# Kernel tuning notes

Measured on AMD Instinct MI355X. Metric: run time of the kernel, lower is better.

The kernel has to match this reference:

```python
import jax, jax.numpy as jnp
import numpy as np
from jax import lax

# Rotation permutations for a flattened 3x3 kernel (row-major, new_flat[t] = orig_flat[perm[t]]),
# transcribed literally from _rotate_kernel for n = angle//45 in {0,1,2,3}.
PERMS = np.array([
    [0, 1, 2, 3, 4, 5, 6, 7, 8],  # 0 deg (identity)
    [3, 0, 1, 6, 4, 2, 7, 8, 5],  # 45 deg: outer ring shifted one step
    [6, 3, 0, 7, 4, 1, 8, 5, 2],  # 90 deg clockwise
    [7, 6, 3, 8, 4, 0, 5, 2, 1],  # 135 deg
], dtype=np.int32)


def setup_inputs() -> dict:
    key = jax.random.key(0)
    k1, k2, k3 = jax.random.split(key, 3)
    B, Cin, Cout, H, W = 16, 64, 64, 128, 128
    x = jax.random.normal(k1, (B, Cin, H, W), dtype=jnp.float32)
    weight = jax.random.normal(k2, (Cout, Cin, 3, 3), dtype=jnp.float32)
    bias = jax.random.normal(k3, (Cout, 1, 1), dtype=jnp.float32)
    return {"x": x, "weight": weight, "bias": bias}


def reference(x, weight, bias):
    # x: [B, Cin, H, W]; weight: [Cout, Cin, 3, 3]; bias: [Cout, 1, 1]
    B, Cin, H, W = x.shape
    Cout = weight.shape[0]
    n_ang = PERMS.shape[0]

    # Build the 4 rotated kernel variants in one gather.
    wflat = weight.reshape(Cout, Cin, 9)
    # [Cout, Cin, n_ang, 9] -> [n_ang, Cout, Cin, 3, 3] -> merge angle into output channels
    wrot = wflat[:, :, jnp.asarray(PERMS)].transpose(2, 0, 1, 3).reshape(n_ang * Cout, Cin, 3, 3)

    # ZeroPad2d(stride=1) then valid 3x3 conv -> same spatial size.
    xp = jnp.pad(x, ((0, 0), (0, 0), (1, 1), (1, 1)))
    y = lax.conv_general_dilated(
        xp, wrot, window_strides=(1, 1), padding="VALID",
        dimension_numbers=("NCHW", "OIHW", "NCHW"))  # [B, n_ang*Cout, H, W]

    y = y.reshape(B, n_ang, Cout, H, W).transpose(1, 0, 2, 3, 4)  # [n_ang, B, Cout, H, W]
    return y + bias  # bias (Cout,1,1) broadcasts over trailing dims
```

## Files before the change

kernel.cpp:

```cpp
#include <hip/hip_runtime.h>


#define CIN 64
#define COUT 64
#define HH 128
#define WW 128
#define NB 16

typedef short bf16x8 __attribute__((ext_vector_type(8)));
typedef float f32x16 __attribute__((ext_vector_type(16)));

#define XS_SLOT 1072
#define XS_ROW  8576
#define XS_OFF  73728
#define LDS_BYTES (XS_OFF + 4 * XS_ROW)

__device__ __constant__ unsigned BOFF_d[4][9] = {
  {0,16,32,8576,8592,8608,17152,17168,17184},
  {16,32,8608,0,8592,17184,8576,17152,17168},
  {32,8608,17184,16,8592,17168,0,8576,17152},
  {8608,17184,17168,32,8592,17152,16,0,8576},
};

static __device__ __forceinline__ unsigned short f2bf(float f) {
  unsigned u = __builtin_bit_cast(unsigned, f);
  unsigned r = (u + 0x7FFFu + ((u >> 16) & 1u)) >> 16;
  return (unsigned short)r;
}

__global__ void build_A_kernel(const float* __restrict__ wgt,
                               unsigned short* __restrict__ A) {
  const int e = blockIdx.x * 256 + threadIdx.x;
  const int j = e & 7;
  const int cm = (e >> 3) & 63;
  const int half = (e >> 9) & 1;
  const int kc = e >> 10;
  const int s = kc >> 2, q = kc & 3;
  const int ci = q * 16 + half * 8 + j;
  A[e] = f2bf(wgt[(cm * CIN + ci) * 9 + s]);
}

__global__ __launch_bounds__(512) void aconv_persist_kernel(
    const float* __restrict__ x,
    const unsigned short* __restrict__ Ag,
    const float* __restrict__ bias,
    float* __restrict__ out)
{
  __shared__ __align__(16) unsigned char lds[LDS_BYTES];

  const int tid = threadIdx.x;
  const int lane = tid & 63;
  const int wid = tid >> 6;
  const int a   = wid >> 1;
  const int row = wid & 1;
  const int half = lane >> 5;
  const int ln = lane & 31;

  const int blk = blockIdx.x;
  const int b   = blk >> 4;
  const int rem = blk & 15;

  float bv[2][16];
  #pragma unroll
  for (int mf = 0; mf < 2; ++mf)
    #pragma unroll
    for (int g = 0; g < 16; ++g)
      bv[mf][g] = bias[mf * 32 + (g & 3) + 8 * (g >> 2) + 4 * half];

  unsigned boff[9];
  #pragma unroll
  for (int s = 0; s < 9; ++s) boff[s] = BOFF_d[a][s];

  {
    const uint4* Ag4 = (const uint4*)Ag;
    uint4* As4 = (uint4*)lds;
    #pragma unroll
    for (int i = 0; i < 9; ++i)
      As4[tid + i * 512] = Ag4[tid + i * 512];
  }

  int grr[5], gwI[5]; unsigned gdst[5]; const float* gxb[5];
  #pragma unroll
  for (int i = 0; i < 5; ++i) {
    const int g = tid + i * 512;
    const int gg = (g < 2112) ? g : 0;
    const int r = gg / 528;
    const int rest = gg - r * 528;
    const int slot = rest / 66;
    const int wI = rest - slot * 66;
    grr[i] = r; gwI[i] = wI;
    gdst[i] = (unsigned)(r * XS_ROW + slot * XS_SLOT + wI * 16);
    gxb[i] = x + (size_t)(b * CIN + slot * 8) * (HH * WW);
  }

  float gxv[5][8];

  {
    const int h0 = (rem * 4) * 2;
    const int w0 = 0;
    #pragma unroll
    for (int i = 0; i < 5; ++i) {
      const int g = tid + i * 512;
      const int gh = h0 - 1 + grr[i];
      const int gw = w0 - 1 + gwI[i];
      const bool inb = (g < 2112) && (gh >= 0) && (gh < HH) && (gw >= 0) && (gw < WW);
      const float* xp = gxb[i] + gh * WW + gw;
      #pragma unroll
      for (int q = 0; q < 8; ++q)
        gxv[i][q] = inb ? xp[q * (HH * WW)] : 0.f;
    }
    #pragma unroll
    for (int i = 0; i < 5; ++i)
      if (tid + i * 512 < 2112) {
        uint4 u4;
        u4.x = (unsigned)f2bf(gxv[i][0]) | ((unsigned)f2bf(gxv[i][1]) << 16);
        u4.y = (unsigned)f2bf(gxv[i][2]) | ((unsigned)f2bf(gxv[i][3]) << 16);
        u4.z = (unsigned)f2bf(gxv[i][4]) | ((unsigned)f2bf(gxv[i][5]) << 16);
        u4.w = (unsigned)f2bf(gxv[i][6]) | ((unsigned)f2bf(gxv[i][7]) << 16);
        *(uint4*)(lds + XS_OFF + gdst[i]) = u4;
      }
  }
  __syncthreads();

  const unsigned char* Asb = lds + (unsigned)(half * 1024 + ln * 16);
  const unsigned char* Bsb = lds + XS_OFF + (unsigned)(row * XS_ROW + half * XS_SLOT + ln * 16);

  for (int it = 0; it < 8; ++it) {
    const int h0 = (rem * 4 + (it >> 1)) * 2;
    const int w0 = (it & 1) * 64;

    if (it < 7) {
      const int itn = it + 1;
      const int h0n = (rem * 4 + (itn >> 1)) * 2;
      const int w0n = (itn & 1) * 64;
      #pragma unroll
      for (int i = 0; i < 5; ++i) {
        const int g = tid + i * 512;
        const int gh = h0n - 1 + grr[i];
        const int gw = w0n - 1 + gwI[i];
        const bool inb = (g < 2112) && (gh >= 0) && (gh < HH) && (gw >= 0) && (gw < WW);
        const float* xp = gxb[i] + gh * WW + gw;
        #pragma unroll
        for (int q = 0; q < 8; ++q)
          gxv[i][q] = inb ? xp[q * (HH * WW)] : 0.f;
      }
    }

    f32x16 acc[2][2];
    #pragma unroll
    for (int mf = 0; mf < 2; ++mf)
      #pragma unroll
      for (int nf = 0; nf < 2; ++nf)
        #pragma unroll
        for (int g = 0; g < 16; ++g)
          acc[mf][nf][g] = bv[mf][g];

    #pragma unroll
    for (int kc = 0; kc < 36; ++kc) {
      const int s = kc >> 2, q = kc & 3;
      const bf16x8 af0 = *(const bf16x8*)(Asb + kc * 2048);
      const bf16x8 af1 = *(const bf16x8*)(Asb + kc * 2048 + 512);
      const unsigned bb = boff[s] + (unsigned)(q * 2 * XS_SLOT);
      const bf16x8 bf0 = *(const bf16x8*)(Bsb + bb);
      const bf16x8 bf1 = *(const bf16x8*)(Bsb + bb + 512);
      acc[0][0] = __builtin_amdgcn_mfma_f32_32x32x16_bf16(af0, bf0, acc[0][0], 0, 0, 0);
      acc[0][1] = __builtin_amdgcn_mfma_f32_32x32x16_bf16(af0, bf1, acc[0][1], 0, 0, 0);
      acc[1][0] = __builtin_amdgcn_mfma_f32_32x32x16_bf16(af1, bf0, acc[1][0], 0, 0, 0);
      acc[1][1] = __builtin_amdgcn_mfma_f32_32x32x16_bf16(af1, bf1, acc[1][1], 0, 0, 0);
    }

    #pragma unroll
    for (int mf = 0; mf < 2; ++mf)
      #pragma unroll
      for (int nf = 0; nf < 2; ++nf) {
        const f32x16 v = acc[mf][nf];
        float* op = out + (((size_t)(a * NB + b) * COUT + mf * 32 + 4 * half) * HH
                           + (h0 + row)) * WW + w0 + nf * 32 + ln;
        #pragma unroll
        for (int g = 0; g < 16; ++g) {
          const int rowc = (g & 3) + 8 * (g >> 2);
          op[(size_t)rowc * (HH * WW)] = v[g];
        }
      }

    __syncthreads();
    if (it < 7) {
      #pragma unroll
      for (int i = 0; i < 5; ++i)
        if (tid + i * 512 < 2112) {
          uint4 u4;
          u4.x = (unsigned)f2bf(gxv[i][0]) | ((unsigned)f2bf(gxv[i][1]) << 16);
          u4.y = (unsigned)f2bf(gxv[i][2]) | ((unsigned)f2bf(gxv[i][3]) << 16);
          u4.z = (unsigned)f2bf(gxv[i][4]) | ((unsigned)f2bf(gxv[i][5]) << 16);
          u4.w = (unsigned)f2bf(gxv[i][6]) | ((unsigned)f2bf(gxv[i][7]) << 16);
          *(uint4*)(lds + XS_OFF + gdst[i]) = u4;
        }
    }
    __syncthreads();
  }
}

extern "C" void kernel_launch(void* const* d_in, const int* in_sizes, int n_in,
                              void* d_out, int out_size, void* d_ws, size_t ws_size,
                              hipStream_t stream) {
  const float* x    = (const float*)d_in[0];
  const float* wgt  = (const float*)d_in[1];
  const float* bias = (const float*)d_in[2];
  float* out = (float*)d_out;
  unsigned short* A = (unsigned short*)d_ws;

  build_A_kernel<<<144, 256, 0, stream>>>(wgt, A);
  aconv_persist_kernel<<<256, 512, 0, stream>>>(x, A, bias, out);
}
```

Before: 107.7 us.

## Widen conv tile to full 128-column rows with split prefetch and lighter barriers

The per-iteration tile grows from 64 to the full 128 columns, so each wave keeps 8 accumulators and each block runs 4 iterations instead of 8. The LDS slot layout is widened, and the zero-padding columns are written once up front. Global loads of the next rows are split into two halves interleaved with the two halves of the MFMA k-loop. Bias is now added at store time, and __syncthreads is replaced by an LDS-only waitcnt plus s_barrier. This aims to cut halo overhead, barrier count and load latency exposure, at the cost of more accumulator registers and lower occupancy.

Result: slower. 160.8 us (+49.3%).

```diff
diff --git a/kernel.cpp b/kernel.cpp
--- a/kernel.cpp
+++ b/kernel.cpp
@@ -6,26 +6,29 @@
 #define HH 128
 #define WW 128
 #define NB 16
+#define HW (HH*WW)
 
 typedef short bf16x8 __attribute__((ext_vector_type(8)));
 typedef float f32x16 __attribute__((ext_vector_type(16)));
 
-#define XS_SLOT 1072
-#define XS_ROW  8576
+#define XS_SLOT 2096
+#define XS_ROW  16768
 #define XS_OFF  73728
 #define LDS_BYTES (XS_OFF + 4 * XS_ROW)
 
 __device__ __constant__ unsigned BOFF_d[4][9] = {
-  {0,16,32,8576,8592,8608,17152,17168,17184},
-  {16,32,8608,0,8592,17184,8576,17152,17168},
-  {32,8608,17184,16,8592,17168,0,8576,17152},
-  {8608,17184,17168,32,8592,17152,16,0,8576},
+  {0,16,32,16768,16784,16800,33536,33552,33568},
+  {16,32,16800,0,16784,33568,16768,33536,33552},
+  {32,16800,33568,16,16784,33552,0,16768,33536},
+  {16800,33568,33552,32,16784,33536,16,0,16768},
 };
 
 static __device__ __forceinline__ unsigned short f2bf(float f) {
   unsigned u = __builtin_bit_cast(unsigned, f);
-  unsigned r = (u + 0x7FFFu + ((u >> 16) & 1u)) >> 16;
-  return (unsigned short)r;
+  return (unsigned short)((u + 0x7FFFu + ((u >> 16) & 1u)) >> 16);
+}
+static __device__ __forceinline__ unsigned pk2(float lo, float hi) {
+  return (unsigned)f2bf(lo) | ((unsigned)f2bf(hi) << 16);
 }
 
 __global__ void build_A_kernel(const float* __restrict__ wgt,
@@ -40,7 +43,12 @@
   A[e] = f2bf(wgt[(cm * CIN + ci) * 9 + s]);
 }
 
-__global__ __launch_bounds__(512) void aconv_persist_kernel(
+static __device__ __forceinline__ void lgkm_barrier() {
+  asm volatile("s_waitcnt lgkmcnt(0)" ::: "memory");
+  __builtin_amdgcn_s_barrier();
+}
+
+__global__ __launch_bounds__(512) void aconv_v6_kernel(
     const float* __restrict__ x,
     const unsigned short* __restrict__ Ag,
     const float* __restrict__ bias,
@@ -59,13 +67,7 @@
   const int blk = blockIdx.x;
   const int b   = blk >> 4;
   const int rem = blk & 15;
-
-  float bv[2][16];
-  #pragma unroll
-  for (int mf = 0; mf < 2; ++mf)
-    #pragma unroll
-    for (int g = 0; g < 16; ++g)
-      bv[mf][g] = bias[mf * 32 + (g & 3) + 8 * (g >> 2) + 4 * half];
+  const int hbase = rem * 8;
 
   unsigned boff[9];
   #pragma unroll
@@ -75,128 +77,146 @@
     const uint4* Ag4 = (const uint4*)Ag;
     uint4* As4 = (uint4*)lds;
     #pragma unroll
-    for (int i = 0; i < 9; ++i)
-      As4[tid + i * 512] = Ag4[tid + i * 512];
-  }
-
-  int grr[5], gwI[5]; unsigned gdst[5]; const float* gxb[5];
+    for (int i = 0; i < 9; ++i) As4[tid + i * 512] = Ag4[tid + i * 512];
+  }
+  if (tid < 64) {
+    const int r = tid >> 4, slot = (tid >> 1) & 7, wI = (tid & 1) * 129;
+    uint4 z = {0u, 0u, 0u, 0u};
+    *(uint4*)(lds + XS_OFF + r * XS_ROW + slot * XS_SLOT + wI * 16) = z;
+  }
+
+  const int sslot = tid >> 7;
+  const int scol  = tid & 127;
+  const float* xb[2];
+  xb[0] = x + (size_t)(b * CIN + sslot * 8) * HW + scol;
+  xb[1] = x + (size_t)(b * CIN + (4 + sslot) * 8) * HW + scol;
+  unsigned sdst[8];
   #pragma unroll
-  for (int i = 0; i < 5; ++i) {
-    const int g = tid + i * 512;
-    const int gg = (g < 2112) ? g : 0;
-    const int r = gg / 528;
-    const int rest = gg - r * 528;
-    const int slot = rest / 66;
-    const int wI = rest - slot * 66;
-    grr[i] = r; gwI[i] = wI;
-    gdst[i] = (unsigned)(r * XS_ROW + slot * XS_SLOT + wI * 16);
-    gxb[i] = x + (size_t)(b * CIN + slot * 8) * (HH * WW);
-  }
-
-  float gxv[5][8];
+  for (int i = 0; i < 8; ++i)
+    sdst[i] = (unsigned)(XS_OFF + (i >> 1) * XS_ROW + ((i & 1) * 4 + sslot) * XS_SLOT
+                         + (1 + scol) * 16);
 
   {
-    const int h0 = (rem * 4) * 2;
-    const int w0 = 0;
-    #pragma unroll
-    for (int i = 0; i < 5; ++i) {
-      const int g = tid + i * 512;
-      const int gh = h0 - 1 + grr[i];
-      const int gw = w0 - 1 + gwI[i];
-      const bool inb = (g < 2112) && (gh >= 0) && (gh < HH) && (gw >= 0) && (gw < WW);
-      const float* xp = gxb[i] + gh * WW + gw;
-      #pragma unroll
-      for (int q = 0; q < 8; ++q)
-        gxv[i][q] = inb ? xp[q * (HH * WW)] : 0.f;
-    }
-    #pragma unroll
-    for (int i = 0; i < 5; ++i)
-      if (tid + i * 512 < 2112) {
-        uint4 u4;
-        u4.x = (unsigned)f2bf(gxv[i][0]) | ((unsigned)f2bf(gxv[i][1]) << 16);
-        u4.y = (unsigned)f2bf(gxv[i][2]) | ((unsigned)f2bf(gxv[i][3]) << 16);
-        u4.z = (unsigned)f2bf(gxv[i][4]) | ((unsigned)f2bf(gxv[i][5]) << 16);
-        u4.w = (unsigned)f2bf(gxv[i][6]) | ((unsigned)f2bf(gxv[i][7]) << 16);
-        *(uint4*)(lds + XS_OFF + gdst[i]) = u4;
-      }
+    float gv[8][8];
+    #pragma unroll
+    for (int i = 0; i < 8; ++i) {
+      const int gh = hbase - 1 + (i >> 1);
+      const bool inb = (unsigned)gh < HH;
+      const float* xp = xb[i & 1] + (size_t)gh * WW;
+      #pragma unroll
+      for (int q = 0; q < 8; ++q) gv[i][q] = inb ? xp[(size_t)q * HW] : 0.f;
+    }
+    #pragma unroll
+    for (int i = 0; i < 8; ++i) {
+      uint4 u;
+      u.x = pk2(gv[i][0], gv[i][1]); u.y = pk2(gv[i][2], gv[i][3]);
+      u.z = pk2(gv[i][4], gv[i][5]); u.w = pk2(gv[i][6], gv[i][7]);
+      *(uint4*)(lds + sdst[i]) = u;
+    }
   }
   __syncthreads();
 
   const unsigned char* Asb = lds + (unsigned)(half * 1024 + ln * 16);
   const unsigned char* Bsb = lds + XS_OFF + (unsigned)(row * XS_ROW + half * XS_SLOT + ln * 16);
 
-  for (int it = 0; it < 8; ++it) {
-    const int h0 = (rem * 4 + (it >> 1)) * 2;
-    const int w0 = (it & 1) * 64;
-
-    if (it < 7) {
-      const int itn = it + 1;
-      const int h0n = (rem * 4 + (itn >> 1)) * 2;
-      const int w0n = (itn & 1) * 64;
-      #pragma unroll
-      for (int i = 0; i < 5; ++i) {
-        const int g = tid + i * 512;
-        const int gh = h0n - 1 + grr[i];
-        const int gw = w0n - 1 + gwI[i];
-        const bool inb = (g < 2112) && (gh >= 0) && (gh < HH) && (gw >= 0) && (gw < WW);
-        const float* xp = gxb[i] + gh * WW + gw;
-        #pragma unroll
-        for (int q = 0; q < 8; ++q)
-          gxv[i][q] = inb ? xp[q * (HH * WW)] : 0.f;
-      }
-    }
-
-    f32x16 acc[2][2];
+  #pragma unroll 1
+  for (int it = 0; it < 4; ++it) {
+    const int h0 = hbase + it * 2;
+    const bool pf = (it < 3);
+
+    f32x16 acc[2][4];
     #pragma unroll
     for (int mf = 0; mf < 2; ++mf)
       #pragma unroll
-      for (int nf = 0; nf < 2; ++nf)
-        #pragma unroll
-        for (int g = 0; g < 16; ++g)
-          acc[mf][nf][g] = bv[mf][g];
-
-    #pragma unroll
-    for (int kc = 0; kc < 36; ++kc) {
+      for (int wq = 0; wq < 4; ++wq) acc[mf][wq] = (f32x16)(0.f);
+
+    auto kstep = [&](int kc) {
       const int s = kc >> 2, q = kc & 3;
       const bf16x8 af0 = *(const bf16x8*)(Asb + kc * 2048);
       const bf16x8 af1 = *(const bf16x8*)(Asb + kc * 2048 + 512);
       const unsigned bb = boff[s] + (unsigned)(q * 2 * XS_SLOT);
-      const bf16x8 bf0 = *(const bf16x8*)(Bsb + bb);
-      const bf16x8 bf1 = *(const bf16x8*)(Bsb + bb + 512);
-      acc[0][0] = __builtin_amdgcn_mfma_f32_32x32x16_bf16(af0, bf0, acc[0][0], 0, 0, 0);
-      acc[0][1] = __builtin_amdgcn_mfma_f32_32x32x16_bf16(af0, bf1, acc[0][1], 0, 0, 0);
-      acc[1][0] = __builtin_amdgcn_mfma_f32_32x32x16_bf16(af1, bf0, acc[1][0], 0, 0, 0);
-      acc[1][1] = __builtin_amdgcn_mfma_f32_32x32x16_bf16(af1, bf1, acc[1][1], 0, 0, 0);
-    }
-
-    #pragma unroll
-    for (int mf = 0; mf < 2; ++mf)
-      #pragma unroll
-      for (int nf = 0; nf < 2; ++nf) {
-        const f32x16 v = acc[mf][nf];
-        float* op = out + (((size_t)(a * NB + b) * COUT + mf * 32 + 4 * half) * HH
-                           + (h0 + row)) * WW + w0 + nf * 32 + ln;
+      bf16x8 bfv[4];
+      #pragma unroll
+      for (int wq = 0; wq < 4; ++wq)
+        bfv[wq] = *(const bf16x8*)(Bsb + bb + wq * 512);
+      #pragma unroll
+      for (int wq = 0; wq < 4; ++wq) {
+        acc[0][wq] = __builtin_amdgcn_mfma_f32_32x32x16_bf16(af0, bfv[wq], acc[0][wq], 0, 0, 0);
+        acc[1][wq] = __builtin_amdgcn_mfma_f32_32x32x16_bf16(af1, bfv[wq], acc[1][wq], 0, 0, 0);
+      }
+    };
+
+    float gA[4][8];
+    if (pf) {
+      #pragma unroll
+      for (int i = 0; i < 4; ++i) {
+        const int gh = h0 + 1 + (i >> 1);
+        const bool inb = (unsigned)gh < HH;
+        const float* xp = xb[i & 1] + (size_t)gh * WW;
         #pragma unroll
-        for (int g = 0; g < 16; ++g) {
-          const int rowc = (g & 3) + 8 * (g >> 2);
-          op[(size_t)rowc * (HH * WW)] = v[g];
-        }
-      }
-
-    __syncthreads();
-    if (it < 7) {
-      #pragma unroll
-      for (int i = 0; i < 5; ++i)
-        if (tid + i * 512 < 2112) {
-          uint4 u4;
-          u4.x = (unsigned)f2bf(gxv[i][0]) | ((unsigned)f2bf(gxv[i][1]) << 16);
-          u4.y = (unsigned)f2bf(gxv[i][2]) | ((unsigned)f2bf(gxv[i][3]) << 16);
-          u4.z = (unsigned)f2bf(gxv[i][4]) | ((unsigned)f2bf(gxv[i][5]) << 16);
-          u4.w = (unsigned)f2bf(gxv[i][6]) | ((unsigned)f2bf(gxv[i][7]) << 16);
-          *(uint4*)(lds + XS_OFF + gdst[i]) = u4;
-        }
-    }
-    __syncthreads();
+        for (int q = 0; q < 8; ++q) gA[i][q] = inb ? xp[(size_t)q * HW] : 0.f;
+      }
+    }
+
+    #pragma unroll
+    for (int kc = 0; kc < 18; ++kc) kstep(kc);
+
+    uint4 gpA[4];
+    float gB[4][8];
+    if (pf) {
+      #pragma unroll
+      for (int i = 0; i < 4; ++i) {
+        gpA[i].x = pk2(gA[i][0], gA[i][1]); gpA[i].y = pk2(gA[i][2], gA[i][3]);
+        gpA[i].z = pk2(gA[i][4], gA[i][5]); gpA[i].w = pk2(gA[i][6], gA[i][7]);
+      }
+      #pragma unroll
+      for (int i = 0; i < 4; ++i) {
+        const int gh = h0 + 3 + (i >> 1);
+        const bool inb = (unsigned)gh < HH;
+        const float* xp = xb[i & 1] + (size_t)gh * WW;
+        #pragma unroll
+        for (int q = 0; q < 8; ++q) gB[i][q] = inb ? xp[(size_t)q * HW] : 0.f;
+      }
+    }
+
+    #pragma unroll
+    for (int kc = 18; kc < 36; ++kc) kstep(kc);
+
+    uint4 gpB[4];
+    if (pf) {
+      #pragma unroll
+      for (int i = 0; i < 4; ++i) {
+        gpB[i].x = pk2(gB[i][0], gB[i][1]); gpB[i].y = pk2(gB[i][2], gB[i][3]);
+        gpB[i].z = pk2(gB[i][4], gB[i][5]); gpB[i].w = pk2(gB[i][6], gB[i][7]);
+      }
+    }
+
+    #pragma unroll
+    for (int mf = 0; mf < 2; ++mf) {
+      const int cob = mf * 32 + 4 * half;
+      float bvl[16];
+      #pragma unroll
+      for (int g = 0; g < 16; ++g)
+        bvl[g] = bias[cob + (g & 3) + 8 * (g >> 2)];
+      #pragma unroll
+      for (int wq = 0; wq < 4; ++wq) {
+        const f32x16 v = acc[mf][wq];
+        float* op = out + (((size_t)(a * NB + b) * COUT + cob) * HH + (h0 + row)) * WW
+                    + wq * 32 + ln;
+        #pragma unroll
+        for (int g = 0; g < 16; ++g)
+          op[(size_t)((g & 3) + 8 * (g >> 2)) * HW] = v[g] + bvl[g];
+      }
+    }
+
+    lgkm_barrier();
+    if (pf) {
+      #pragma unroll
+      for (int i = 0; i < 4; ++i) *(uint4*)(lds + sdst[i]) = gpA[i];
+      #pragma unroll
+      for (int i = 0; i < 4; ++i) *(uint4*)(lds + sdst[4 + i]) = gpB[i];
+    }
+    lgkm_barrier();
   }
 }
 
@@ -210,5 +230,5 @@
   unsigned short* A = (unsigned short*)d_ws;
 
   build_A_kernel<<<144, 256, 0, stream>>>(wgt, A);
-  aconv_persist_kernel<<<256, 512, 0, stream>>>(x, A, bias, out);
-}
+  aconv_v6_kernel<<<256, 512, 0, stream>>>(x, A, bias, out);
+}
```

## Reuse halo rows via 4-slot ring buffer, nontemporal output stores

Applied to the files above, without the earlier changes.

Changes the tile traversal so each block walks down 8 rows of one 64-wide column half, keeping a 4-row circular LDS buffer. Only the two new input rows are loaded per step instead of all four, which roughly halves redundant global loads and bf16 conversions. Per-tile B offsets are recomputed from the row-rotation table. Output stores become nontemporal, and __syncthreads is replaced by a lgkmcnt wait plus s_barrier. The cost is more complex indexing and extra per-iteration offset math.

Measured after the change: 101.3 us. -5.9%, faster.

```diff
diff --git a/kernel.cpp b/kernel.cpp
--- a/kernel.cpp
+++ b/kernel.cpp
@@ -6,6 +6,7 @@
 #define HH 128
 #define WW 128
 #define NB 16
+#define HW (HH*WW)
 
 typedef short bf16x8 __attribute__((ext_vector_type(8)));
 typedef float f32x16 __attribute__((ext_vector_type(16)));
@@ -15,17 +16,25 @@
 #define XS_OFF  73728
 #define LDS_BYTES (XS_OFF + 4 * XS_ROW)
 
-__device__ __constant__ unsigned BOFF_d[4][9] = {
-  {0,16,32,8576,8592,8608,17152,17168,17184},
-  {16,32,8608,0,8592,17184,8576,17152,17168},
-  {32,8608,17184,16,8592,17168,0,8576,17152},
-  {8608,17184,17168,32,8592,17152,16,0,8576},
+__device__ __constant__ unsigned char DHI_d[4][9] = {
+  {0,0,0,1,1,1,2,2,2},
+  {0,0,1,0,1,2,1,2,2},
+  {0,1,2,0,1,2,0,1,2},
+  {1,2,2,0,1,2,0,0,1},
+};
+__device__ __constant__ unsigned short DWB_d[4][9] = {
+  {0,16,32,0,16,32,0,16,32},
+  {16,32,32,0,16,32,0,0,16},
+  {32,32,32,16,16,16,0,0,0},
+  {32,32,16,32,16,0,16,0,0},
 };
 
 static __device__ __forceinline__ unsigned short f2bf(float f) {
   unsigned u = __builtin_bit_cast(unsigned, f);
-  unsigned r = (u + 0x7FFFu + ((u >> 16) & 1u)) >> 16;
-  return (unsigned short)r;
+  return (unsigned short)((u + 0x7FFFu + ((u >> 16) & 1u)) >> 16);
+}
+static __device__ __forceinline__ unsigned pk2(float lo, float hi) {
+  return (unsigned)f2bf(lo) | ((unsigned)f2bf(hi) << 16);
 }
 
 __global__ void build_A_kernel(const float* __restrict__ wgt,
@@ -40,7 +49,12 @@
   A[e] = f2bf(wgt[(cm * CIN + ci) * 9 + s]);
 }
 
-__global__ __launch_bounds__(512) void aconv_persist_kernel(
+static __device__ __forceinline__ void lgkm_barrier() {
+  asm volatile("s_waitcnt lgkmcnt(0)" ::: "memory");
+  __builtin_amdgcn_s_barrier();
+}
+
+__global__ __launch_bounds__(512) void aconv_v7_kernel(
     const float* __restrict__ x,
     const unsigned short* __restrict__ Ag,
     const float* __restrict__ bias,
@@ -59,6 +73,7 @@
   const int blk = blockIdx.x;
   const int b   = blk >> 4;
   const int rem = blk & 15;
+  const int hbase = rem * 8;
 
   float bv[2][16];
   #pragma unroll
@@ -67,82 +82,89 @@
     for (int g = 0; g < 16; ++g)
       bv[mf][g] = bias[mf * 32 + (g & 3) + 8 * (g >> 2) + 4 * half];
 
-  unsigned boff[9];
-  #pragma unroll
-  for (int s = 0; s < 9; ++s) boff[s] = BOFF_d[a][s];
+  int dhi[9]; unsigned dwb[9];
+  #pragma unroll
+  for (int s = 0; s < 9; ++s) { dhi[s] = DHI_d[a][s]; dwb[s] = DWB_d[a][s]; }
 
   {
     const uint4* Ag4 = (const uint4*)Ag;
     uint4* As4 = (uint4*)lds;
     #pragma unroll
-    for (int i = 0; i < 9; ++i)
-      As4[tid + i * 512] = Ag4[tid + i * 512];
+    for (int i = 0; i < 9; ++i) As4[tid + i * 512] = Ag4[tid + i * 512];
   }
 
-  int grr[5], gwI[5]; unsigned gdst[5]; const float* gxb[5];
+  float gv[5][8];
+  unsigned gdst[5];
+  bool gval[5];
+
   #pragma unroll
   for (int i = 0; i < 5; ++i) {
     const int g = tid + i * 512;
-    const int gg = (g < 2112) ? g : 0;
-    const int r = gg / 528;
-    const int rest = gg - r * 528;
+    const bool v = g < 2112;
+    const int rg = g / 528;
+    const int rest = g - rg * 528;
     const int slot = rest / 66;
     const int wI = rest - slot * 66;
-    grr[i] = r; gwI[i] = wI;
-    gdst[i] = (unsigned)(r * XS_ROW + slot * XS_SLOT + wI * 16);
-    gxb[i] = x + (size_t)(b * CIN + slot * 8) * (HH * WW);
+    const int hx = hbase - 1 + rg;
+    const int gw = -1 + wI;
+    const bool inb = v && ((unsigned)hx < HH) && ((unsigned)gw < WW);
+    const float* xp = x + (size_t)(b * CIN + slot * 8) * HW + (size_t)hx * WW + gw;
+    gval[i] = v;
+    gdst[i] = (unsigned)(XS_OFF + rg * XS_ROW + slot * XS_SLOT + wI * 16);
+    #pragma unroll
+    for (int q = 0; q < 8; ++q) gv[i][q] = inb ? xp[(size_t)q * HW] : 0.f;
   }
-
-  float gxv[5][8];
-
-  {
-    const int h0 = (rem * 4) * 2;
-    const int w0 = 0;
-    #pragma unroll
-    for (int i = 0; i < 5; ++i) {
-      const int g = tid + i * 512;
-      const int gh = h0 - 1 + grr[i];
-      const int gw = w0 - 1 + gwI[i];
-      const bool inb = (g < 2112) && (gh >= 0) && (gh < HH) && (gw >= 0) && (gw < WW);
-      const float* xp = gxb[i] + gh * WW + gw;
-      #pragma unroll
-      for (int q = 0; q < 8; ++q)
-        gxv[i][q] = inb ? xp[q * (HH * WW)] : 0.f;
-    }
-    #pragma unroll
-    for (int i = 0; i < 5; ++i)
-      if (tid + i * 512 < 2112) {
-        uint4 u4;
-        u4.x = (unsigned)f2bf(gxv[i][0]) | ((unsigned)f2bf(gxv[i][1]) << 16);
-        u4.y = (unsigned)f2bf(gxv[i][2]) | ((unsigned)f2bf(gxv[i][3]) << 16);
-        u4.z = (unsigned)f2bf(gxv[i][4]) | ((unsigned)f2bf(gxv[i][5]) << 16);
-        u4.w = (unsigned)f2bf(gxv[i][6]) | ((unsigned)f2bf(gxv[i][7]) << 16);
-        *(uint4*)(lds + XS_OFF + gdst[i]) = u4;
-      }
-  }
+  #pragma unroll
+  for (int i = 0; i < 5; ++i)
+    if (gval[i]) {
+      uint4 u;
+      u.x = pk2(gv[i][0], gv[i][1]); u.y = pk2(gv[i][2], gv[i][3]);
+      u.z = pk2(gv[i][4], gv[i][5]); u.w = pk2(gv[i][6], gv[i][7]);
+      *(uint4*)(lds + gdst[i]) = u;
+    }
   __syncthreads();
 
   const unsigned char* Asb = lds + (unsigned)(half * 1024 + ln * 16);
-  const unsigned char* Bsb = lds + XS_OFF + (unsigned)(row * XS_ROW + half * XS_SLOT + ln * 16);
-
-  for (int it = 0; it < 8; ++it) {
-    const int h0 = (rem * 4 + (it >> 1)) * 2;
-    const int w0 = (it & 1) * 64;
-
-    if (it < 7) {
-      const int itn = it + 1;
-      const int h0n = (rem * 4 + (itn >> 1)) * 2;
-      const int w0n = (itn & 1) * 64;
+  const unsigned char* Bsb = lds + XS_OFF + (unsigned)(half * XS_SLOT + ln * 16);
+
+  #pragma unroll 1
+  for (int ti = 0; ti < 8; ++ti) {
+    const int wh = ti >> 2, it = ti & 3;
+    const int w0 = wh * 64;
+
+    unsigned boff_t[9];
+    {
+      unsigned rowoff[3];
+      #pragma unroll
+      for (int dh = 0; dh < 3; ++dh)
+        rowoff[dh] = (unsigned)(((2 * it + row + dh) & 3) * XS_ROW);
+      #pragma unroll
+      for (int s = 0; s < 9; ++s) boff_t[s] = dwb[s] + rowoff[dhi[s]];
+    }
+
+    const bool pf2 = (it < 3);
+    const bool pf4 = (it == 3) && (wh == 0);
+    const int ngran = pf2 ? 1056 : (pf4 ? 2112 : 0);
+    if (ngran) {
+      const int itv = pf4 ? -2 : it;
+      const int w0n = pf4 ? 64 : w0;
       #pragma unroll
       for (int i = 0; i < 5; ++i) {
         const int g = tid + i * 512;
-        const int gh = h0n - 1 + grr[i];
-        const int gw = w0n - 1 + gwI[i];
-        const bool inb = (g < 2112) && (gh >= 0) && (gh < HH) && (gw >= 0) && (gw < WW);
-        const float* xp = gxb[i] + gh * WW + gw;
+        const bool v = g < ngran;
+        const int rg = g / 528;
+        const int rest = g - rg * 528;
+        const int slot = rest / 66;
+        const int wI = rest - slot * 66;
+        const int hx = hbase + 2 * itv + 3 + rg;
+        const int ps = (2 * itv + 4 + rg) & 3;
+        const int gw = w0n - 1 + wI;
+        const bool inb = v && ((unsigned)hx < HH) && ((unsigned)gw < WW);
+        const float* xp = x + (size_t)(b * CIN + slot * 8) * HW + (size_t)hx * WW + gw;
+        gval[i] = v;
+        gdst[i] = (unsigned)(XS_OFF + ps * XS_ROW + slot * XS_SLOT + wI * 16);
         #pragma unroll
-        for (int q = 0; q < 8; ++q)
-          gxv[i][q] = inb ? xp[q * (HH * WW)] : 0.f;
+        for (int q = 0; q < 8; ++q) gv[i][q] = inb ? xp[(size_t)q * HW] : 0.f;
       }
     }
 
@@ -157,10 +179,9 @@
 
     #pragma unroll
     for (int kc = 0; kc < 36; ++kc) {
-      const int s = kc >> 2, q = kc & 3;
       const bf16x8 af0 = *(const bf16x8*)(Asb + kc * 2048);
       const bf16x8 af1 = *(const bf16x8*)(Asb + kc * 2048 + 512);
-      const unsigned bb = boff[s] + (unsigned)(q * 2 * XS_SLOT);
+      const unsigned bb = boff_t[kc >> 2] + (unsigned)((kc & 3) * 2 * XS_SLOT);
       const bf16x8 bf0 = *(const bf16x8*)(Bsb + bb);
       const bf16x8 bf1 = *(const bf16x8*)(Bsb + bb + 512);
       acc[0][0] = __builtin_amdgcn_mfma_f32_32x32x16_bf16(af0, bf0, acc[0][0], 0, 0, 0);
@@ -169,34 +190,31 @@
       acc[1][1] = __builtin_amdgcn_mfma_f32_32x32x16_bf16(af1, bf1, acc[1][1], 0, 0, 0);
     }
 
+    const int hout = hbase + it * 2 + row;
     #pragma unroll
     for (int mf = 0; mf < 2; ++mf)
       #pragma unroll
       for (int nf = 0; nf < 2; ++nf) {
         const f32x16 v = acc[mf][nf];
         float* op = out + (((size_t)(a * NB + b) * COUT + mf * 32 + 4 * half) * HH
-                           + (h0 + row)) * WW + w0 + nf * 32 + ln;
+                           + hout) * WW + w0 + nf * 32 + ln;
         #pragma unroll
-        for (int g = 0; g < 16; ++g) {
-          const int rowc = (g & 3) + 8 * (g >> 2);
-          op[(size_t)rowc * (HH * WW)] = v[g];
+        for (int g = 0; g < 16; ++g)
+          __builtin_nontemporal_store(v[g], op + (size_t)((g & 3) + 8 * (g >> 2)) * HW);
+      }
+
+    lgkm_barrier();
+    if (ngran) {
+      #pragma unroll
+      for (int i = 0; i < 5; ++i)
+        if (gval[i]) {
+          uint4 u;
+          u.x = pk2(gv[i][0], gv[i][1]); u.y = pk2(gv[i][2], gv[i][3]);
+          u.z = pk2(gv[i][4], gv[i][5]); u.w = pk2(gv[i][6], gv[i][7]);
+          *(uint4*)(lds + gdst[i]) = u;
         }
-      }
-
-    __syncthreads();
-    if (it < 7) {
-      #pragma unroll
-      for (int i = 0; i < 5; ++i)
-        if (tid + i * 512 < 2112) {
-          uint4 u4;
-          u4.x = (unsigned)f2bf(gxv[i][0]) | ((unsigned)f2bf(gxv[i][1]) << 16);
-          u4.y = (unsigned)f2bf(gxv[i][2]) | ((unsigned)f2bf(gxv[i][3]) << 16);
-          u4.z = (unsigned)f2bf(gxv[i][4]) | ((unsigned)f2bf(gxv[i][5]) << 16);
-          u4.w = (unsigned)f2bf(gxv[i][6]) | ((unsigned)f2bf(gxv[i][7]) << 16);
-          *(uint4*)(lds + XS_OFF + gdst[i]) = u4;
-        }
-    }
-    __syncthreads();
+    }
+    lgkm_barrier();
   }
 }
 
@@ -210,5 +228,5 @@
   unsigned short* A = (unsigned short*)d_ws;
 
   build_A_kernel<<<144, 256, 0, stream>>>(wgt, A);
-  aconv_persist_kernel<<<256, 512, 0, stream>>>(x, A, bias, out);
-}
+  aconv_v7_kernel<<<256, 512, 0, stream>>>(x, A, bias, out);
+}
```
